# Performance work log

Measured on AMD Instinct MI355X. Metric: run time of the kernel, lower is better.

Reference implementation:

```python
import jax, jax.numpy as jnp
import numpy as np

G, N, E = 16, 512, 2048        # graphs, nodes/graph, edges/graph
CN, CE = 64, 64                # node / edge feature channels
K = 3                          # Laguerre polynomial order
RATIO = 0.5
KEEP = int(np.ceil(RATIO * N)) # 256 kept nodes per graph (static)
POWER_ITERS = 64               # power iteration approximating eigsh(k=1,'LM')


def setup_inputs() -> dict:
    key = jax.random.key(0)
    ks = jax.random.split(key, 10)
    x_n = jax.random.normal(ks[0], (G * N, CN), jnp.float32)
    x_e = jax.random.normal(ks[1], (G * E, CE), jnp.float32)
    # incidence endpoints per edge, local node ids, no self loops
    u = jax.random.randint(ks[2], (G, E), 0, N)
    v = (u + 1 + jax.random.randint(ks[3], (G, E), 0, N - 1)) % N
    # node-level conv graph (global ids within per-graph blocks): both directions
    offs = (jnp.arange(G) * N)[:, None]
    src_n = jnp.concatenate([(u + offs).reshape(-1), (v + offs).reshape(-1)])
    dst_n = jnp.concatenate([(v + offs).reshape(-1), (u + offs).reshape(-1)])
    edge_weight_n = jax.random.uniform(ks[4], (src_n.shape[0],), jnp.float32)
    # edge-level conv graph (global ids within per-graph edge blocks)
    ME = 4 * E
    offs_e = (jnp.arange(G) * E)[:, None]
    src_e = (jax.random.randint(ks[5], (G, ME), 0, E) + offs_e).reshape(-1)
    dst_e = (jax.random.randint(ks[6], (G, ME), 0, E) + offs_e).reshape(-1)
    edge_weight_e = jax.random.uniform(ks[7], (src_e.shape[0],), jnp.float32)
    # HodgeLaguerreConv(C -> 1, K) weights (glorot-ish) + bias (zeros init)
    W_n = jax.random.normal(ks[8], (K, CN), jnp.float32) / np.sqrt(CN)
    b_n = jnp.zeros((1,), jnp.float32)
    W_e = jax.random.normal(ks[9], (K, CE), jnp.float32) / np.sqrt(CE)
    b_e = jnp.zeros((1,), jnp.float32)
    return dict(x_n=x_n, x_e=x_e, edge_u=u, edge_v=v,
                src_n=src_n, dst_n=dst_n, edge_weight_n=edge_weight_n,
                src_e=src_e, dst_e=dst_e, edge_weight_e=edge_weight_e,
                W_n=W_n, b_n=b_n, W_e=W_e, b_e=b_e)


def hodge_laguerre(x, src, dst, w, Wk, b):
    """HodgeLaguerreConv with out_channels=1: out = sum_k T_k(L) x @ Wk[k] + b.
    T_0 = x; T_1 = x - Lx; T_{k+1} = (-L T_k + (2k+1) T_k - k T_{k-1})/(k+1)."""
    num = x.shape[0]
    def L(z):  # scatter-add message passing: out[i] = sum_{j->i} norm * z[j]
        return jax.ops.segment_sum(w[:, None] * z[src], dst, num_segments=num)
    Tx0 = x
    out = Tx0 @ Wk[0]
    Tx1 = x - L(x)
    out = out + Tx1 @ Wk[1]
    k = 1
    for i in range(2, Wk.shape[0]):
        Tx2 = (-L(Tx1) + (2 * k + 1) * Tx1 - k * Tx0) / (k + 1)
        out = out + Tx2 @ Wk[i]
        Tx0, Tx1 = Tx1, Tx2
        k += 1
    return out + b[0]


def pool_graph(sn, se, xn, xe, u, v):
    # node score augmented by |B1| @ edge_score (abs incidence gathers both endpoints)
    aug = sn.at[u].add(se).at[v].add(se)
    perm = jnp.argsort(-aug)                    # descending sort, take top KEEP
    mask_n = jnp.zeros((N,), xn.dtype).at[perm[:KEEP]].set(1.0)
    # mask_e = |B1|^T (1 - mask_n); keep edge iff both endpoints kept (== 0)
    bad = (1.0 - mask_n[u]) + (1.0 - mask_n[v])
    keep_e = (bad == 0.0).astype(xn.dtype)
    # dense incidence B1 [N, E]: -1 at source row, +1 at target row
    cols = jnp.arange(E)
    B = jnp.zeros((N, E), xn.dtype).at[u, cols].add(-1.0).at[v, cols].add(1.0)
    Bm = B * mask_n[:, None] * keep_e[None, :]  # row/col masking (zero-padded)
    L0 = Bm @ Bm.T                              # [N, N] node Laplacian
    L1 = Bm.T @ Bm                              # [E, E] edge Laplacian
    # power iteration for lambda_max(L0) (== eigsh k=1 'LM'; zero rows keep spectrum)
    w = jnp.ones((N,), xn.dtype) / np.sqrt(N)
    for _ in range(POWER_ITERS):
        w = L0 @ w
        w = w / (jnp.linalg.norm(w) + 1e-12)
    lam = w @ (L0 @ w)
    scale = 2.0 / (lam + 1e-12)
    return xn * mask_n[:, None], L0 * scale, xe * keep_e[:, None], L1 * scale


def reference(x_n, x_e, edge_u, edge_v, src_n, dst_n, edge_weight_n,
              src_e, dst_e, edge_weight_e, W_n, b_n, W_e, b_e):
    score_n = jax.nn.sigmoid(hodge_laguerre(x_n, src_n, dst_n, edge_weight_n, W_n, b_n).reshape(-1))
    score_e = jax.nn.sigmoid(hodge_laguerre(x_e, src_e, dst_e, edge_weight_e, W_e, b_e).reshape(-1))
    xn_g = (x_n * score_n[:, None]).reshape(G, N, CN)
    xe_g = (x_e * score_e[:, None]).reshape(G, E, CE)
    sn = score_n.reshape(G, N)
    se = score_e.reshape(G, E)
    return jax.vmap(pool_graph)(sn, se, xn_g, xe_g, edge_u, edge_v)
```

## Files before the change

### kernel.cpp

```cpp
#include <hip/hip_runtime.h>
#include <math.h>

#define GG 16
#define NNODE 512
#define EEDGE 2048
#define KEEPN 256
#define PITERS 64
#define NNT 8192
#define NET 32768

typedef float vfloat4 __attribute__((ext_vector_type(4)));

#define WS_C1N 0
#define WS_C2N 8192
#define WS_BN  16384
#define WS_C1E 24576
#define WS_C2E 57344
#define WS_BE  90112
#define WS_SNW 122880
#define WS_SEW 131072
#define WS_KLIST 163840
#define WS_KCNT 196608
#define WS_SCALE 196624

#define O_XN 0
#define O_L0 524288
#define O_XE 4718592
#define O_L1 6815744

#define AC_D1N 0
#define AC_D2N 8192
#define AC_E2N 16384
#define AC_D1E 24576
#define AC_D2E 57344
#define AC_E2E 90112
#define AC_TOT4 30720

#define L04 1048576
#define ZTOT4 17825792

#define DCAP 12

__global__ __launch_bounds__(512) void k_dots(
    const float* __restrict__ xn, const float* __restrict__ xe,
    const float* __restrict__ Wn, const float* __restrict__ We,
    float* __restrict__ ws, float* __restrict__ out) {
  const int tid = threadIdx.x, bid = blockIdx.x;
  if (bid >= 1024) {
    vfloat4 z = (vfloat4)(0.f);
    vfloat4* a4 = (vfloat4*)(out + O_L0);
    int base = (bid - 1024) * 512 + tid;
    #pragma unroll
    for (int k = 0; k < 4; ++k) a4[base + k * 7680] = z;
    return;
  }
  const int lane = tid & 63;
  const int wv = (bid * 512 + tid) >> 6;
  #pragma unroll
  for (int n = 0; n < 5; ++n) {
    int gw = wv + n * 8192;
    const float* x; const float* W; int row; float *c1, *c2, *bs;
    if (gw < NNT) {
      row = gw; x = xn + (size_t)row * 64; W = Wn;
      c1 = ws + WS_C1N; c2 = ws + WS_C2N; bs = ws + WS_BN;
    } else {
      row = gw - NNT;
      x = xe + (size_t)row * 64; W = We;
      c1 = ws + WS_C1E; c2 = ws + WS_C2E; bs = ws + WS_BE;
    }
    float v = x[lane];
    float r0 = v * W[lane];
    float r1 = v * W[64 + lane];
    float r2 = v * W[128 + lane];
    for (int o = 32; o; o >>= 1) {
      r0 += __shfl_xor(r0, o, 64);
      r1 += __shfl_xor(r1, o, 64);
      r2 += __shfl_xor(r2, o, 64);
    }
    if (lane == 0) { c1[row] = r1; c2[row] = r2; bs[row] = r0 + r1 + r2; }
  }
}

__global__ __launch_bounds__(512) void k_mp1(
    const int* __restrict__ src_n, const int* __restrict__ dst_n, const float* __restrict__ wn,
    const int* __restrict__ src_e, const int* __restrict__ dst_e, const float* __restrict__ we,
    const float* __restrict__ ws, float* __restrict__ out) {
  int gid = blockIdx.x * 512 + threadIdx.x;
  float* acc = (float*)(out + O_L0);
  if (gid < 65536) {
    int s = src_n[gid], d = dst_n[gid]; float w = wn[gid];
    atomicAdd(&acc[AC_D1N + d], w * ws[WS_C1N + s]);
    atomicAdd(&acc[AC_D2N + d], w * ws[WS_C2N + s]);
  } else {
    int e = gid - 65536;
    int s = src_e[e], d = dst_e[e]; float w = we[e];
    atomicAdd(&acc[AC_D1E + d], w * ws[WS_C1E + s]);
    atomicAdd(&acc[AC_D2E + d], w * ws[WS_C2E + s]);
  }
}

__global__ __launch_bounds__(512) void k_mp2(
    const int* __restrict__ src_n, const int* __restrict__ dst_n, const float* __restrict__ wn,
    const int* __restrict__ src_e, const int* __restrict__ dst_e, const float* __restrict__ we,
    float* __restrict__ out) {
  int gid = blockIdx.x * 512 + threadIdx.x;
  float* acc = (float*)(out + O_L0);
  if (gid < 65536) {
    int s = src_n[gid], d = dst_n[gid]; float w = wn[gid];
    atomicAdd(&acc[AC_E2N + d], w * acc[AC_D2N + s]);
  } else {
    int e = gid - 65536;
    int s = src_e[e], d = dst_e[e]; float w = we[e];
    atomicAdd(&acc[AC_E2E + d], w * acc[AC_D2E + s]);
  }
}

#define PM_AUG  0
#define PM_RED  512
#define PM_IWS  520
#define PM_KCP  528
#define PM_MASK 544
#define PM_DEG  1056
#define PM_OFF  1568
#define PM_SUV  2080
#define PM_ADJ  4128
#define PM_WVA  6176
#define PM_WVB  6692
#define PM_TOT  7208
__global__ __launch_bounds__(512, 2) void k_pool(
    const int* __restrict__ edge_u, const int* __restrict__ edge_v,
    const float* __restrict__ bnp, const float* __restrict__ bep,
    float* __restrict__ ws, float* __restrict__ out) {
  const int tid = threadIdx.x;
  if (blockIdx.x >= 16) {
    vfloat4 z = (vfloat4)(0.f);
    vfloat4* o4 = (vfloat4*)out;
    int base = (blockIdx.x - 16) * 512 + tid;
    #pragma unroll
    for (int n = 0; n < 17; ++n) {
      int i = AC_TOT4 + base + n * 1048576;
      if (i < ZTOT4) {
        int f = (i < L04) ? (O_L0 / 4 + i) : (O_L1 / 4 + (i - L04));
        __builtin_nontemporal_store(z, &o4[f]);
      }
    }
    return;
  }
  __shared__ float smem[PM_TOT];
  int* smi = (int*)smem;
  float* aug = smem + PM_AUG;
  float* red = smem + PM_RED;
  int* iws   = smi + PM_IWS;
  int* kcp   = smi + PM_KCP;
  int* maskS = smi + PM_MASK;
  int* degS  = smi + PM_DEG;
  int* offS  = smi + PM_OFF;
  int* suv   = smi + PM_SUV;
  unsigned short* adjU = (unsigned short*)(smi + PM_ADJ);
  float* wvA = smem + PM_WVA;
  float* wvB = smem + PM_WVB;

  const int g = blockIdx.x;
  const int roffN = g * NNODE;
  const int roffE = g * EEDGE;
  const int lane = tid & 63, wid = tid >> 6;
  const float* acc = (const float*)(out + O_L0);
  float biasN = bnp[0], biasE = bep[0];

  float bn  = ws[WS_BN + roffN + tid];
  float nd1 = acc[AC_D1N + roffN + tid];
  float nd2 = acc[AC_D2N + roffN + tid];
  float ne2 = acc[AC_E2N + roffN + tid];
  float beR[4], d1R[4], d2R[4], e2R[4]; int uR[4], vR[4];
  #pragma unroll
  for (int n = 0; n < 4; ++n) {
    int e = roffE + tid + n * 512;
    beR[n] = ws[WS_BE + e];
    d1R[n] = acc[AC_D1E + e];
    d2R[n] = acc[AC_D2E + e];
    e2R[n] = acc[AC_E2E + e];
    uR[n] = edge_u[e];
    vR[n] = edge_v[e];
  }

  float tn = bn - nd1 - 2.0f * nd2 + 0.5f * ne2 + biasN;
  float snw_r = 1.0f / (1.0f + expf(-tn));
  aug[tid] = snw_r;
  degS[tid] = 0;
  if (tid == 0) *kcp = 0;
  __syncthreads();

  float seR[4];
  #pragma unroll
  for (int n = 0; n < 4; ++n) {
    float te = beR[n] - d1R[n] - 2.0f * d2R[n] + 0.5f * e2R[n] + biasE;
    float s = 1.0f / (1.0f + expf(-te));
    seR[n] = s;
    atomicAdd(&aug[uR[n]], s);
    atomicAdd(&aug[vR[n]], s);
  }
  __syncthreads();

  {
    float a = aug[tid];
    int r = 0;
    #pragma unroll 8
    for (int j = 0; j < NNODE; ++j) {
      float b = aug[j];
      r += (b > a) || (b == a && j < tid);
    }
    maskS[tid] = (r < KEEPN) ? 1 : 0;
  }
  __syncthreads();
  ws[WS_SNW + roffN + tid] = snw_r * (float)maskS[tid];

  int* wsi = (int*)ws;
  #pragma unroll
  for (int n = 0; n < 4; ++n) {
    int e = tid + n * 512;
    int u = uR[n], v = vR[n];
    suv[e] = u | (v << 16);
    int k = maskS[u] & maskS[v];
    ws[WS_SEW + roffE + e] = seR[n] * (float)k;
    if (k) {
      int p = atomicAdd(kcp, 1);
      wsi[WS_KLIST + roffE + p] = e;
      atomicAdd(&degS[u], 1);
      atomicAdd(&degS[v], 1);
    }
  }
  __syncthreads();
  if (tid == 0) wsi[WS_KCNT + g] = *kcp;

  int dv = degS[tid];
  int inc = dv;
  for (int o = 1; o < 64; o <<= 1) {
    int t = __shfl_up(inc, o, 64);
    if (lane >= o) inc += t;
  }
  if (lane == 63) iws[wid] = inc;
  __syncthreads();
  int base = 0;
  for (int k = 0; k < wid; ++k) base += iws[k];
  int myStart = base + inc - dv;
  offS[tid] = myStart;
  __syncthreads();

  for (int e = tid; e < EEDGE; e += 512) {
    int p2 = suv[e];
    int u = p2 & 0xffff, v = p2 >> 16;
    if (maskS[u] & maskS[v]) {
      int pu = atomicAdd(&offS[u], 1); adjU[pu] = (unsigned short)v;
      int pv = atomicAdd(&offS[v], 1); adjU[pv] = (unsigned short)u;
    }
  }
  __syncthreads();
  int myDeg = dv;
  int myEnd = myStart + myDeg;

  int nbr[DCAP];
  #pragma unroll
  for (int k = 0; k < DCAP; ++k)
    nbr[k] = (k < myDeg) ? (int)adjU[myStart + k] : NNODE;
  bool ovf = myDeg > DCAP;

  wvA[tid] = 0.04419417382415922f;
  if (tid == 0) { wvA[NNODE] = 0.f; wvB[NNODE] = 0.f; }
  __syncthreads();
  float* wcur = wvA; float* wnext = wvB;
  for (int it = 0; it < PITERS; ++it) {
    float tg[DCAP];
    #pragma unroll
    for (int k = 0; k < DCAP; ++k) tg[k] = wcur[nbr[k]];
    float acc2 = (float)myDeg * wcur[tid];
    #pragma unroll
    for (int k = 0; k < DCAP; ++k) acc2 -= tg[k];
    if (ovf) for (int p = myStart + DCAP; p < myEnd; ++p) acc2 -= wcur[(int)adjU[p]];
    if ((it & 7) == 7) {
      float sq = acc2 * acc2;
      for (int o = 32; o; o >>= 1) sq += __shfl_xor(sq, o, 64);
      if (lane == 0) red[wid] = sq;
      __syncthreads();
      float tot = red[0] + red[1] + red[2] + red[3]
                + red[4] + red[5] + red[6] + red[7];
      wnext[tid] = acc2 * (1.0f / (sqrtf(tot) + 1e-12f));
    } else {
      wnext[tid] = acc2;
    }
    __syncthreads();
    float* tmp = wcur; wcur = wnext; wnext = tmp;
  }
  {
    float tg[DCAP];
    #pragma unroll
    for (int k = 0; k < DCAP; ++k) tg[k] = wcur[nbr[k]];
    float wv_ = wcur[tid];
    float acc2 = (float)myDeg * wv_;
    #pragma unroll
    for (int k = 0; k < DCAP; ++k) acc2 -= tg[k];
    if (ovf) for (int p = myStart + DCAP; p < myEnd; ++p) acc2 -= wcur[(int)adjU[p]];
    float pr = wv_ * acc2;
    for (int o = 32; o; o >>= 1) pr += __shfl_xor(pr, o, 64);
    if (lane == 0) red[wid] = pr;
    __syncthreads();
    if (tid == 0) {
      float lam = red[0] + red[1] + red[2] + red[3]
                + red[4] + red[5] + red[6] + red[7];
      ws[WS_SCALE + g] = 2.0f / (lam + 1e-12f);
    }
  }
}

__global__ __launch_bounds__(256) void k_out(
    const float* __restrict__ xn, const float* __restrict__ xe,
    const int* __restrict__ edge_u, const int* __restrict__ edge_v,
    const float* __restrict__ ws, float* __restrict__ out) {
  int b = blockIdx.x, tid = threadIdx.x;
  const int* wsi = (const int*)ws;
  if (b < 512) {
    int idx = b * 256 + tid;
    int row = idx >> 4;
    float s = ws[WS_SNW + row];
    float4 x4 = ((const float4*)xn)[idx];
    ((float4*)(out + O_XN))[idx] = make_float4(x4.x * s, x4.y * s, x4.z * s, x4.w * s);
  } else if (b < 2560) {
    int idx = (b - 512) * 256 + tid;
    int row = idx >> 4;
    float s = ws[WS_SEW + row];
    float4 x4 = ((const float4*)xe)[idx];
    ((float4*)(out + O_XE))[idx] = make_float4(x4.x * s, x4.y * s, x4.z * s, x4.w * s);
  } else if (b < 2576) {
    int g = b - 2560;
    if (g == 0) {
      float4 z4 = make_float4(0.f, 0.f, 0.f, 0.f);
      float4* a4 = (float4*)(out + O_L0);
      for (int i = tid; i < AC_TOT4; i += 256) a4[i] = z4;
      __syncthreads();
    }
    int cnt = wsi[WS_KCNT + g];
    float s = ws[WS_SCALE + g];
    float* L0 = out + O_L0 + (long long)g * (NNODE * NNODE);
    const int* kl = wsi + WS_KLIST + g * EEDGE;
    const int* eu = edge_u + g * EEDGE;
    const int* ev = edge_v + g * EEDGE;
    for (int t = tid; t < cnt; t += 256) {
      int e = kl[t];
      int u = eu[e], v = ev[e];
      atomicAdd(&L0[u * NNODE + u], s);
      atomicAdd(&L0[v * NNODE + v], s);
      atomicAdd(&L0[u * NNODE + v], -s);
      atomicAdd(&L0[v * NNODE + u], -s);
    }
  } else {
    int q = b - 2576;
    int g = q >> 8, sb = q & 255;
    int cnt = wsi[WS_KCNT + g];
    float s = ws[WS_SCALE + g];
    float* L1 = out + O_L1 + (long long)g * (EEDGE * EEDGE);
    const int* kl = wsi + WS_KLIST + g * EEDGE;
    const int* eu = edge_u + g * EEDGE;
    const int* ev = edge_v + g * EEDGE;
    for (int a = sb; a < cnt; a += 256) {
      int e1 = kl[a];
      int u1 = eu[e1], v1 = ev[e1];
      long long rowoff = (long long)e1 * EEDGE;
      for (int b2 = tid; b2 < cnt; b2 += 256) {
        int e2 = kl[b2];
        int u2 = eu[e2], v2 = ev[e2];
        int val = (u1 == u2) + (v1 == v2) - (v1 == u2) - (u1 == v2);
        if (val) L1[rowoff + e2] = s * (float)val;
      }
    }
  }
}

extern "C" void kernel_launch(void* const* d_in, const int* in_sizes, int n_in,
                              void* d_out, int out_size, void* d_ws, size_t ws_size,
                              hipStream_t stream) {
  const float* x_n = (const float*)d_in[0];
  const float* x_e = (const float*)d_in[1];
  const int* edge_u = (const int*)d_in[2];
  const int* edge_v = (const int*)d_in[3];
  const int* src_n = (const int*)d_in[4];
  const int* dst_n = (const int*)d_in[5];
  const float* ew_n = (const float*)d_in[6];
  const int* src_e = (const int*)d_in[7];
  const int* dst_e = (const int*)d_in[8];
  const float* ew_e = (const float*)d_in[9];
  const float* W_n = (const float*)d_in[10];
  const float* b_n = (const float*)d_in[11];
  const float* W_e = (const float*)d_in[12];
  const float* b_e = (const float*)d_in[13];
  float* ws = (float*)d_ws;
  float* out = (float*)d_out;

  k_dots<<<1024 + 15, 512, 0, stream>>>(x_n, x_e, W_n, W_e, ws, out);
  k_mp1<<<384, 512, 0, stream>>>(src_n, dst_n, ew_n, src_e, dst_e, ew_e, ws, out);
  k_mp2<<<384, 512, 0, stream>>>(src_n, dst_n, ew_n, src_e, dst_e, ew_e, out);
  k_pool<<<16 + 2048, 512, 0, stream>>>(edge_u, edge_v, b_n, b_e, ws, out);
  k_out<<<6672, 256, 0, stream>>>(x_n, x_e, edge_u, edge_v, ws, out);
}
```

Before: 416.2 us.

## Spread output zero-fill across mp1, mp2 and pool kernels; unroll power iteration

The large zero-fill of the L0/L1 output region, previously done entirely by extra blocks of the pooling kernel, is split into three ranges handled by extra blocks appended to k_mp1, k_mp2 and k_pool. The aim is to hide store bandwidth behind the latency-bound atomic scatter kernels and shorten the pool kernel's tail. The power iteration is also unrolled by two with fixed buffers to remove pointer swapping. The risk is that the extra blocks compete with the atomics, and the manual range arithmetic must cover every element exactly once.

```diff
diff --git a/kernel.cpp b/kernel.cpp
--- a/kernel.cpp
+++ b/kernel.cpp
@@ -38,6 +38,9 @@
 
 #define L04 1048576
 #define ZTOT4 17825792
+#define Z_MP1_LO (AC_TOT4)
+#define Z_MP2_LO (AC_TOT4 + 3932160)
+#define Z_POOL_LO (AC_TOT4 + 7864320)
 
 #define DCAP 12
 
@@ -85,7 +88,20 @@
     const int* __restrict__ src_n, const int* __restrict__ dst_n, const float* __restrict__ wn,
     const int* __restrict__ src_e, const int* __restrict__ dst_e, const float* __restrict__ we,
     const float* __restrict__ ws, float* __restrict__ out) {
-  int gid = blockIdx.x * 512 + threadIdx.x;
+  const int tid = threadIdx.x, bid = blockIdx.x;
+  if (bid >= 384) {
+    vfloat4 z = (vfloat4)(0.f);
+    vfloat4* o4 = (vfloat4*)out;
+    int base = Z_MP1_LO + (bid - 384) * 512 + tid;
+    #pragma unroll
+    for (int n = 0; n < 12; ++n) {
+      int i = base + n * 327680;
+      int f = (i < L04) ? (O_L0 / 4 + i) : (O_L1 / 4 + (i - L04));
+      __builtin_nontemporal_store(z, &o4[f]);
+    }
+    return;
+  }
+  int gid = bid * 512 + tid;
   float* acc = (float*)(out + O_L0);
   if (gid < 65536) {
     int s = src_n[gid], d = dst_n[gid]; float w = wn[gid];
@@ -103,7 +119,20 @@
     const int* __restrict__ src_n, const int* __restrict__ dst_n, const float* __restrict__ wn,
     const int* __restrict__ src_e, const int* __restrict__ dst_e, const float* __restrict__ we,
     float* __restrict__ out) {
-  int gid = blockIdx.x * 512 + threadIdx.x;
+  const int tid = threadIdx.x, bid = blockIdx.x;
+  if (bid >= 384) {
+    vfloat4 z = (vfloat4)(0.f);
+    vfloat4* o4 = (vfloat4*)out;
+    int base = Z_MP2_LO + (bid - 384) * 512 + tid;
+    #pragma unroll
+    for (int n = 0; n < 12; ++n) {
+      int i = base + n * 327680;
+      int f = (i < L04) ? (O_L0 / 4 + i) : (O_L1 / 4 + (i - L04));
+      __builtin_nontemporal_store(z, &o4[f]);
+    }
+    return;
+  }
+  int gid = bid * 512 + tid;
   float* acc = (float*)(out + O_L0);
   if (gid < 65536) {
     int s = src_n[gid], d = dst_n[gid]; float w = wn[gid];
@@ -127,6 +156,31 @@
 #define PM_WVA  6176
 #define PM_WVB  6692
 #define PM_TOT  7208
+
+#define POWER_STEP(WCUR, WNEXT, IT)                                        \
+  {                                                                        \
+    float tg[DCAP];                                                        \
+    _Pragma("unroll")                                                      \
+    for (int k = 0; k < DCAP; ++k) tg[k] = WCUR[nbr[k]];                   \
+    float acc2 = (float)myDeg * WCUR[tid];                                 \
+    _Pragma("unroll")                                                      \
+    for (int k = 0; k < DCAP; ++k) acc2 -= tg[k];                          \
+    if (ovf) for (int p = myStart + DCAP; p < myEnd; ++p)                  \
+      acc2 -= WCUR[(int)adjU[p]];                                          \
+    if (((IT) & 7) == 7) {                                                 \
+      float sq = acc2 * acc2;                                              \
+      for (int o = 32; o; o >>= 1) sq += __shfl_xor(sq, o, 64);            \
+      if (lane == 0) red[wid] = sq;                                        \
+      __syncthreads();                                                     \
+      float tot = red[0] + red[1] + red[2] + red[3]                        \
+                + red[4] + red[5] + red[6] + red[7];                       \
+      WNEXT[tid] = acc2 * (1.0f / (sqrtf(tot) + 1e-12f));                  \
+    } else {                                                               \
+      WNEXT[tid] = acc2;                                                   \
+    }                                                                      \
+    __syncthreads();                                                       \
+  }
+
 __global__ __launch_bounds__(512, 2) void k_pool(
     const int* __restrict__ edge_u, const int* __restrict__ edge_v,
     const float* __restrict__ bnp, const float* __restrict__ bep,
@@ -135,10 +189,10 @@
   if (blockIdx.x >= 16) {
     vfloat4 z = (vfloat4)(0.f);
     vfloat4* o4 = (vfloat4*)out;
-    int base = (blockIdx.x - 16) * 512 + tid;
-    #pragma unroll
-    for (int n = 0; n < 17; ++n) {
-      int i = AC_TOT4 + base + n * 1048576;
+    int base = Z_POOL_LO + (blockIdx.x - 16) * 512 + tid;
+    #pragma unroll
+    for (int n = 0; n < 10; ++n) {
+      int i = base + n * 1048576;
       if (i < ZTOT4) {
         int f = (i < L04) ? (O_L0 / 4 + i) : (O_L1 / 4 + (i - L04));
         __builtin_nontemporal_store(z, &o4[f]);
@@ -267,38 +321,19 @@
   wvA[tid] = 0.04419417382415922f;
   if (tid == 0) { wvA[NNODE] = 0.f; wvB[NNODE] = 0.f; }
   __syncthreads();
-  float* wcur = wvA; float* wnext = wvB;
-  for (int it = 0; it < PITERS; ++it) {
-    float tg[DCAP];
-    #pragma unroll
-    for (int k = 0; k < DCAP; ++k) tg[k] = wcur[nbr[k]];
-    float acc2 = (float)myDeg * wcur[tid];
-    #pragma unroll
-    for (int k = 0; k < DCAP; ++k) acc2 -= tg[k];
-    if (ovf) for (int p = myStart + DCAP; p < myEnd; ++p) acc2 -= wcur[(int)adjU[p]];
-    if ((it & 7) == 7) {
-      float sq = acc2 * acc2;
-      for (int o = 32; o; o >>= 1) sq += __shfl_xor(sq, o, 64);
-      if (lane == 0) red[wid] = sq;
-      __syncthreads();
-      float tot = red[0] + red[1] + red[2] + red[3]
-                + red[4] + red[5] + red[6] + red[7];
-      wnext[tid] = acc2 * (1.0f / (sqrtf(tot) + 1e-12f));
-    } else {
-      wnext[tid] = acc2;
-    }
-    __syncthreads();
-    float* tmp = wcur; wcur = wnext; wnext = tmp;
+  for (int it = 0; it < PITERS; it += 2) {
+    POWER_STEP(wvA, wvB, it);
+    POWER_STEP(wvB, wvA, it + 1);
   }
   {
     float tg[DCAP];
     #pragma unroll
-    for (int k = 0; k < DCAP; ++k) tg[k] = wcur[nbr[k]];
-    float wv_ = wcur[tid];
+    for (int k = 0; k < DCAP; ++k) tg[k] = wvA[nbr[k]];
+    float wv_ = wvA[tid];
     float acc2 = (float)myDeg * wv_;
     #pragma unroll
     for (int k = 0; k < DCAP; ++k) acc2 -= tg[k];
-    if (ovf) for (int p = myStart + DCAP; p < myEnd; ++p) acc2 -= wcur[(int)adjU[p]];
+    if (ovf) for (int p = myStart + DCAP; p < myEnd; ++p) acc2 -= wvA[(int)adjU[p]];
     float pr = wv_ * acc2;
     for (int o = 32; o; o >>= 1) pr += __shfl_xor(pr, o, 64);
     if (lane == 0) red[wid] = pr;
@@ -395,8 +430,8 @@
   float* out = (float*)d_out;
 
   k_dots<<<1024 + 15, 512, 0, stream>>>(x_n, x_e, W_n, W_e, ws, out);
-  k_mp1<<<384, 512, 0, stream>>>(src_n, dst_n, ew_n, src_e, dst_e, ew_e, ws, out);
-  k_mp2<<<384, 512, 0, stream>>>(src_n, dst_n, ew_n, src_e, dst_e, ew_e, out);
+  k_mp1<<<384 + 640, 512, 0, stream>>>(src_n, dst_n, ew_n, src_e, dst_e, ew_e, ws, out);
+  k_mp2<<<384 + 640, 512, 0, stream>>>(src_n, dst_n, ew_n, src_e, dst_e, ew_e, out);
   k_pool<<<16 + 2048, 512, 0, stream>>>(edge_u, edge_v, b_n, b_e, ws, out);
   k_out<<<6672, 256, 0, stream>>>(x_n, x_e, edge_u, edge_v, ws, out);
 }
```

Result: no change. 420.0 us (+0.9%).
